# Kernel optimization log

Measured on AMD Instinct MI355X. Metric: run time of the kernel, lower is better.

## Reference

```python
import jax, jax.numpy as jnp
import numpy as np

NEG_SLOPE = 0.2  # DGL GATConv default negative_slope


def gat_layer(x, W, al, ar, b, src, dst):
    """One DGL-style GATConv layer. x:[N,F], W:[F,H*D], al/ar:[H,D], b:[H*D].
    Returns [N,H,D]."""
    N = x.shape[0]
    H, D = al.shape
    feat = (x @ W).reshape(N, H, D)               # projected features
    el = jnp.einsum('nhd,hd->nh', feat, al)       # src attention term
    er = jnp.einsum('nhd,hd->nh', feat, ar)       # dst attention term
    e = jax.nn.leaky_relu(el[src] + er[dst], NEG_SLOPE)   # [E,H]
    # segment softmax over destination nodes
    m = jax.ops.segment_max(e, dst, num_segments=N)       # [N,H]
    m = jnp.where(jnp.isfinite(m), m, 0.0)                # isolated nodes
    ex = jnp.exp(e - m[dst])                              # [E,H]
    denom = jax.ops.segment_sum(ex, dst, num_segments=N)  # [N,H]
    a = ex / denom[dst]                                   # [E,H]
    msg = a[:, :, None] * feat[src]                       # [E,H,D]
    rst = jax.ops.segment_sum(msg, dst, num_segments=N)   # [N,H,D]
    return rst + b.reshape(1, H, D)


def setup_inputs() -> dict:
    key = jax.random.key(0)
    ks = jax.random.split(key, 10)
    N, E = 100000, 1600000
    F_IN, H1, D1, F_OUT = 128, 8, 16, 64
    HID = H1 * D1  # 128
    features = jax.random.normal(ks[0], (N, F_IN), dtype=jnp.float32)
    src = jax.random.randint(ks[1], (E,), 0, N, dtype=jnp.int32)
    dst = jax.random.randint(ks[2], (E,), 0, N, dtype=jnp.int32)
    edge_type = jax.random.randint(ks[3], (E,), 0, 4, dtype=jnp.int32)
    s1 = 1.0 / np.sqrt(F_IN)
    s2 = 1.0 / np.sqrt(HID)
    w1 = jax.random.normal(ks[4], (F_IN, HID), dtype=jnp.float32) * s1
    al1 = jax.random.normal(ks[5], (H1, D1), dtype=jnp.float32) * 0.1
    ar1 = jax.random.normal(ks[6], (H1, D1), dtype=jnp.float32) * 0.1
    b1 = jnp.zeros((HID,), dtype=jnp.float32)
    w2 = jax.random.normal(ks[7], (HID, F_OUT), dtype=jnp.float32) * s2
    al2 = jax.random.normal(ks[8], (1, F_OUT), dtype=jnp.float32) * 0.1
    ar2 = jax.random.normal(ks[9], (1, F_OUT), dtype=jnp.float32) * 0.1
    b2 = jnp.zeros((F_OUT,), dtype=jnp.float32)
    return dict(features=features, src=src, dst=dst, edge_type=edge_type,
                w1=w1, al1=al1, ar1=ar1, b1=b1,
                w2=w2, al2=al2, ar2=ar2, b2=b2)


def reference(features, src, dst, edge_type, w1, al1, ar1, b1, w2, al2, ar2, b2):
    N = features.shape[0]
    # conv1: [N,H,D] -> flatten heads -> relu
    h = gat_layer(features, w1, al1, ar1, b1, src, dst).reshape(N, -1)
    h = jax.nn.relu(h)
    # conv2: single head -> squeeze -> relu
    h = gat_layer(h, w2, al2, ar2, b2, src, dst)[:, 0, :]
    h = jax.nn.relu(h)
    # dot-product edge predictor (u_dot_v) + sigmoid
    score = jnp.einsum('ed,ed->e', h[src], h[dst])
    return jax.nn.sigmoid(score)
```

## Files before the change

kernel.cpp:

```cpp
#include <hip/hip_runtime.h>
#include <math.h>

#define F_IN 128
#define HID 128
#define H1 8
#define D1 16
#define F_OUT 64

#define BSHIFT 7
#define NPB 128
#define CH 4096
#define CAP 4096

typedef unsigned int uint;
typedef unsigned short ushort;

typedef __bf16 bf16x8 __attribute__((ext_vector_type(8)));
typedef float f32x4 __attribute__((ext_vector_type(4)));
typedef float f32x2 __attribute__((ext_vector_type(2)));

__device__ __forceinline__ float bf2f(ushort u) {
  uint v = ((uint)u) << 16;
  return __builtin_bit_cast(float, v);
}
__device__ __forceinline__ ushort f2bf(float f) {
  uint u = __builtin_bit_cast(uint, f);
  u = (u + 0x7FFFu + ((u >> 16) & 1u)) >> 16;
  return (ushort)u;
}
__device__ __forceinline__ f32x2 bfpair(uint w) {
  f32x2 r;
  r.x = __builtin_bit_cast(float, w << 16);
  r.y = __builtin_bit_cast(float, w & 0xFFFF0000u);
  return r;
}


__global__ __launch_bounds__(256) void bucket_scatter(const int* __restrict__ src,
                                                      const int* __restrict__ dst,
                                                      int* __restrict__ bcursor,
                                                      uint* __restrict__ pairs, int E, int nb) {
  __shared__ int cnt_l[1024], base_l[1024], off_l[1024];
  for (int i = threadIdx.x; i < nb; i += 256) { cnt_l[i] = 0; off_l[i] = 0; }
  __syncthreads();
  int e0 = blockIdx.x * CH;
  int t = threadIdx.x;
#pragma unroll 4
  for (int k = 0; k < CH / 256; ++k) {
    int e = e0 + k * 256 + t;
    if (e < E) atomicAdd(&cnt_l[dst[e] >> BSHIFT], 1);
  }
  __syncthreads();
  for (int i = t; i < nb; i += 256)
    base_l[i] = cnt_l[i] ? atomicAdd(&bcursor[i], cnt_l[i]) : 0;
  __syncthreads();
#pragma unroll 4
  for (int k = 0; k < CH / 256; ++k) {
    int e = e0 + k * 256 + t;
    if (e < E) {
      int d = dst[e], b = d >> BSHIFT;
      int o = base_l[b] + atomicAdd(&off_l[b], 1);
      if (o < CAP) pairs[(size_t)b * CAP + o] = ((uint)(d & (NPB - 1)) << 25) | (uint)src[e];
    }
  }
}

__global__ void scan_buckets(const int* __restrict__ bcursor, int* __restrict__ bbase,
                             int nb, int total) {
  __shared__ int sdata[1024];
  int t = threadIdx.x;
  int v = (t < nb) ? bcursor[t] : 0;
  sdata[t] = v;
  __syncthreads();
  for (int off = 1; off < 1024; off <<= 1) {
    int u = (t >= off) ? sdata[t - off] : 0;
    __syncthreads();
    sdata[t] += u;
    __syncthreads();
  }
  if (t < nb) bbase[t] = sdata[t] - v;
  if (t == 0) bbase[nb] = total;
}

__global__ __launch_bounds__(256) void build_csr(const uint* __restrict__ pairs,
                                                 const int* __restrict__ bcursor,
                                                 const int* __restrict__ bbase,
                                                 int* __restrict__ row_ptr,
                                                 int* __restrict__ src_sorted,
                                                 int nn, int total) {
  __shared__ int h[NPB], pref[NPB];
  int b = blockIdx.x, t = threadIdx.x;
  if (t < NPB) h[t] = 0;
  __syncthreads();
  size_t lo = (size_t)b * CAP;
  int cnt = bcursor[b];
  int csr_base = bbase[b];
  for (int e = t; e < cnt; e += 256) atomicAdd(&h[pairs[lo + e] >> 25], 1);
  __syncthreads();
  if (t < NPB) pref[t] = h[t];
  __syncthreads();
  for (int off = 1; off < NPB; off <<= 1) {
    int v = (t >= off && t < NPB) ? pref[t - off] : 0;
    __syncthreads();
    if (t < NPB) pref[t] += v;
    __syncthreads();
  }
  int node_base = b << BSHIFT;
  int nodes = min(NPB, nn - node_base);
  if (t < nodes) {
    int ex = csr_base + pref[t] - h[t];
    row_ptr[node_base + t] = ex;
    h[t] = ex;
  }
  __syncthreads();
  for (int e = t; e < cnt; e += 256) {
    uint p = pairs[lo + e];
    int pos = atomicAdd(&h[p >> 25], 1);
    src_sorted[pos] = (int)(p & 0x1FFFFFFu);
  }
  if (b == 0 && t == 0) row_ptr[nn] = total;
}


template <int COLS, bool ABF16>
__global__ __launch_bounds__(256) void mfma_gemm(const void* __restrict__ Xv,
                                                 const float* __restrict__ W,
                                                 ushort* __restrict__ Y, int nrows) {
  constexpr int NCT = COLS / 16;
  __shared__ ushort wlds[128 * COLS];
  constexpr int ITER = (128 * COLS) / 512;
#pragma unroll
  for (int it = 0; it < ITER; ++it) {
    int idx = it * 512 + (int)threadIdx.x * 2;
    float2 wv = *(const float2*)(W + idx);
    int k = idx / COLS, c = idx % COLS;
    int t = k >> 5, kb = (k >> 3) & 3, j = k & 7;
    wlds[(((t * NCT + (c >> 4)) * 64) + ((c & 15) | (kb << 4))) * 8 + j] = f2bf(wv.x);
    int c1 = c + 1;
    wlds[(((t * NCT + (c1 >> 4)) * 64) + ((c1 & 15) | (kb << 4))) * 8 + j] = f2bf(wv.y);
  }
  __syncthreads();

  int wid = threadIdx.x >> 6, lane = threadIdx.x & 63;
  long r0 = (long)blockIdx.x * 256 + wid * 64;
  if (r0 >= nrows) return;
  int lr = lane & 15, kb = lane >> 4;
  long ar[4];
#pragma unroll
  for (int mi = 0; mi < 4; ++mi) {
    long r = r0 + mi * 16 + lr;
    ar[mi] = (r < nrows) ? r : (long)(nrows - 1);
  }
  f32x4 acc[4][NCT];
#pragma unroll
  for (int mi = 0; mi < 4; ++mi)
#pragma unroll
    for (int ct = 0; ct < NCT; ++ct) acc[mi][ct] = (f32x4){0.f, 0.f, 0.f, 0.f};

#pragma unroll
  for (int t = 0; t < 4; ++t) {
    bf16x8 af[4];
#pragma unroll
    for (int mi = 0; mi < 4; ++mi) {
      if constexpr (ABF16) {
        const ushort* xp = (const ushort*)Xv + ar[mi] * 128 + t * 32 + kb * 8;
        af[mi] = *(const bf16x8*)xp;
      } else {
        const float* xp = (const float*)Xv + ar[mi] * 128 + t * 32 + kb * 8;
        float4 u = *(const float4*)xp;
        float4 v = *(const float4*)(xp + 4);
        bf16x8 a;
        a[0] = (__bf16)u.x; a[1] = (__bf16)u.y; a[2] = (__bf16)u.z; a[3] = (__bf16)u.w;
        a[4] = (__bf16)v.x; a[5] = (__bf16)v.y; a[6] = (__bf16)v.z; a[7] = (__bf16)v.w;
        af[mi] = a;
      }
    }
#pragma unroll
    for (int ct = 0; ct < NCT; ++ct) {
      bf16x8 bf = *(const bf16x8*)&wlds[((t * NCT + ct) * 64 + lane) * 8];
#pragma unroll
      for (int mi = 0; mi < 4; ++mi)
        acc[mi][ct] = __builtin_amdgcn_mfma_f32_16x16x32_bf16(af[mi], bf, acc[mi][ct], 0, 0, 0);
    }
  }

#pragma unroll
  for (int mi = 0; mi < 4; ++mi) {
#pragma unroll
    for (int ct = 0; ct < NCT; ++ct) {
#pragma unroll
      for (int reg = 0; reg < 4; ++reg) {
        long r = r0 + mi * 16 + kb * 4 + reg;
        if (r < nrows) Y[r * COLS + ct * 16 + lr] = f2bf(acc[mi][ct][reg]);
      }
    }
  }
}


__global__ void elr1_kernel(const ushort* __restrict__ feat, const float* __restrict__ al,
                            const float* __restrict__ ar, ushort* __restrict__ el,
                            float* __restrict__ er, int nn) {
  int idx = blockIdx.x * blockDim.x + threadIdx.x;
  if (idx >= nn * H1) return;
  int n = idx >> 3, h = idx & 7;
  const uint4* f4 = (const uint4*)(feat + (size_t)n * HID + h * D1);
  const float* a = al + h * D1;
  const float* r = ar + h * D1;
  float sl = 0.f, sr = 0.f;
#pragma unroll
  for (int j = 0; j < 2; ++j) {
    uint4 v = f4[j];
    uint ws[4] = {v.x, v.y, v.z, v.w};
#pragma unroll
    for (int k = 0; k < 4; ++k) {
      float f0 = bf2f((ushort)(ws[k] & 0xFFFF));
      float f1 = bf2f((ushort)(ws[k] >> 16));
      int d = j * 8 + k * 2;
      sl += f0 * a[d] + f1 * a[d + 1];
      sr += f0 * r[d] + f1 * r[d + 1];
    }
  }
  el[idx] = f2bf(sl);
  er[idx] = sr;
}

__global__ void elr2_kernel(const ushort* __restrict__ feat, const float* __restrict__ al,
                            const float* __restrict__ ar, float* __restrict__ el,
                            float* __restrict__ er, int nn) {
  int n = blockIdx.x * blockDim.x + threadIdx.x;
  if (n >= nn) return;
  const uint4* f4 = (const uint4*)(feat + (size_t)n * F_OUT);
  float sl = 0.f, sr = 0.f;
#pragma unroll
  for (int j = 0; j < 8; ++j) {
    uint4 v = f4[j];
    uint ws[4] = {v.x, v.y, v.z, v.w};
#pragma unroll
    for (int k = 0; k < 4; ++k) {
      float f0 = bf2f((ushort)(ws[k] & 0xFFFF));
      float f1 = bf2f((ushort)(ws[k] >> 16));
      int d = j * 8 + k * 2;
      sl += f0 * al[d] + f1 * al[d + 1];
      sr += f0 * ar[d] + f1 * ar[d + 1];
    }
  }
  el[n] = sl;
  er[n] = sr;
}


template <int H, int D, int VEC, bool EL_BF16>
__global__ __launch_bounds__(256) void agg_kernel(
    const ushort* __restrict__ feat, const void* __restrict__ elv,
    const float* __restrict__ er, const int* __restrict__ row_ptr,
    const int* __restrict__ src_sorted, const float* __restrict__ bias,
    ushort* __restrict__ out, int nn) {
  constexpr int F = H * D;
  constexpr int LPG = 16;
  constexpr int CHUNK = 32;
  static_assert(F == LPG * VEC, "lane layout");
  int w = threadIdx.x >> 6, lane = threadIdx.x & 63;
  int g = lane >> 4, li = lane & 15;
  int n = blockIdx.x * 16 + w * 4 + g;
  __shared__ float p_sh[4][4][H][CHUNK + 2];
  __shared__ int s_sh[4][4][CHUNK + 2];
  bool node_ok = n < nn;
  int start = 0, deg = 0;
  if (node_ok) {
    start = row_ptr[n];
    deg = row_ptr[n + 1] - start;
  }
  int d0 = li * VEC;
  int h = d0 / D;
  float er_reg[H];
#pragma unroll
  for (int q = 0; q < H; ++q) er_reg[q] = 0.f;
  if (node_ok) {
    if constexpr (H == 8) {
      float4 e0 = *(const float4*)(er + (size_t)n * 8);
      float4 e1 = *(const float4*)(er + (size_t)n * 8 + 4);
      er_reg[0] = e0.x; er_reg[1] = e0.y; er_reg[2] = e0.z; er_reg[3] = e0.w;
      er_reg[4] = e1.x; er_reg[5] = e1.y; er_reg[6] = e1.z; er_reg[7] = e1.w;
    } else {
      er_reg[0] = er[n];
    }
  }
  float L = 0.f;
  f32x2 acc2[VEC / 2];
#pragma unroll
  for (int v = 0; v < VEC / 2; ++v) acc2[v] = (f32x2){0.f, 0.f};

  for (int c0 = 0; c0 < deg; c0 += CHUNK) {
    int cnt = min(CHUNK, deg - c0);
    int e0i = c0 + 2 * li;
    int2 s2 = make_int2(0, 0);
    if (e0i + 1 < deg) s2 = *(const int2*)(src_sorted + start + e0i);
    else if (e0i < deg) s2.x = src_sorted[start + e0i];
    *(int2*)&s_sh[w][g][2 * li] = s2;
#pragma unroll
    for (int half = 0; half < 2; ++half) {
      int s = half ? s2.y : s2.x;
      bool valid = (e0i + half) < deg;
      float p8[H];
      if (valid) {
        if constexpr (H == 8) {
          float ev[8];
          if constexpr (EL_BF16) {
            uint4 q4 = *(const uint4*)((const ushort*)elv + (size_t)s * 8);
            uint qs[4] = {q4.x, q4.y, q4.z, q4.w};
#pragma unroll
            for (int k = 0; k < 4; ++k) {
              f32x2 f = bfpair(qs[k]);
              ev[2 * k] = f.x;
              ev[2 * k + 1] = f.y;
            }
          } else {
            float4 e0 = *(const float4*)((const float*)elv + (size_t)s * 8);
            float4 e1 = *(const float4*)((const float*)elv + (size_t)s * 8 + 4);
            ev[0] = e0.x; ev[1] = e0.y; ev[2] = e0.z; ev[3] = e0.w;
            ev[4] = e1.x; ev[5] = e1.y; ev[6] = e1.z; ev[7] = e1.w;
          }
#pragma unroll
          for (int q = 0; q < 8; ++q) {
            float v = ev[q] + er_reg[q];
            v = v > 0.f ? v : 0.2f * v;
            p8[q] = __expf(v);
          }
        } else {
          float v = ((const float*)elv)[s] + er_reg[0];
          v = v > 0.f ? v : 0.2f * v;
          p8[0] = __expf(v);
        }
      } else {
#pragma unroll
        for (int q = 0; q < H; ++q) p8[q] = 0.f;
      }
#pragma unroll
      for (int q = 0; q < H; ++q) p_sh[w][g][q][2 * li + half] = p8[q];
    }
    __builtin_amdgcn_wave_barrier();
    const ushort* fb = feat + d0;
    int j = 0;
    for (; j + 3 < cnt; j += 4) {
      int sa = s_sh[w][g][j], sb = s_sh[w][g][j + 1];
      int sc = s_sh[w][g][j + 2], sd = s_sh[w][g][j + 3];
      float pa = p_sh[w][g][h][j], pb = p_sh[w][g][h][j + 1];
      float pc = p_sh[w][g][h][j + 2], pd = p_sh[w][g][h][j + 3];
      L += pa + pb + pc + pd;
      f32x2 Pa = {pa, pa}, Pb = {pb, pb}, Pc = {pc, pc}, Pd = {pd, pd};
      if constexpr (VEC == 8) {
        uint4 va = *(const uint4*)(fb + (size_t)sa * F);
        uint4 vb = *(const uint4*)(fb + (size_t)sb * F);
        uint4 vc = *(const uint4*)(fb + (size_t)sc * F);
        uint4 vd = *(const uint4*)(fb + (size_t)sd * F);
        uint wa[4] = {va.x, va.y, va.z, va.w};
        uint wb[4] = {vb.x, vb.y, vb.z, vb.w};
        uint wc[4] = {vc.x, vc.y, vc.z, vc.w};
        uint wd[4] = {vd.x, vd.y, vd.z, vd.w};
#pragma unroll
        for (int k = 0; k < 4; ++k) {
          acc2[k] += Pa * bfpair(wa[k]);
          acc2[k] += Pb * bfpair(wb[k]);
          acc2[k] += Pc * bfpair(wc[k]);
          acc2[k] += Pd * bfpair(wd[k]);
        }
      } else {
        uint2 va = *(const uint2*)(fb + (size_t)sa * F);
        uint2 vb = *(const uint2*)(fb + (size_t)sb * F);
        uint2 vc = *(const uint2*)(fb + (size_t)sc * F);
        uint2 vd = *(const uint2*)(fb + (size_t)sd * F);
        acc2[0] += Pa * bfpair(va.x) + Pb * bfpair(vb.x) + Pc * bfpair(vc.x) + Pd * bfpair(vd.x);
        acc2[1] += Pa * bfpair(va.y) + Pb * bfpair(vb.y) + Pc * bfpair(vc.y) + Pd * bfpair(vd.y);
      }
    }
    for (; j < cnt; ++j) {
      float pj = p_sh[w][g][h][j];
      int sj = s_sh[w][g][j];
      L += pj;
      f32x2 Pj = {pj, pj};
      if constexpr (VEC == 8) {
        uint4 v = *(const uint4*)(fb + (size_t)sj * F);
        uint wv[4] = {v.x, v.y, v.z, v.w};
#pragma unroll
        for (int k = 0; k < 4; ++k) acc2[k] += Pj * bfpair(wv[k]);
      } else {
        uint2 v = *(const uint2*)(fb + (size_t)sj * F);
        acc2[0] += Pj * bfpair(v.x);
        acc2[1] += Pj * bfpair(v.y);
      }
    }
    __builtin_amdgcn_wave_barrier();
  }

  if (!node_ok) return;
  float inv = (L > 0.f) ? 1.f / L : 0.f;
  ushort us[VEC];
#pragma unroll
  for (int v = 0; v < VEC / 2; ++v) {
    us[2 * v] = f2bf(fmaxf(acc2[v].x * inv + bias[d0 + 2 * v], 0.f));
    us[2 * v + 1] = f2bf(fmaxf(acc2[v].y * inv + bias[d0 + 2 * v + 1], 0.f));
  }
  if constexpr (VEC == 4) {
    ushort4 u4 = {us[0], us[1], us[2], us[3]};
    *(ushort4*)&out[(size_t)n * F + d0] = u4;
  } else {
    ushort4 u40 = {us[0], us[1], us[2], us[3]};
    ushort4 u41 = {us[4], us[5], us[6], us[7]};
    *(ushort4*)&out[(size_t)n * F + d0] = u40;
    *(ushort4*)&out[(size_t)n * F + d0 + 4] = u41;
  }
}


__global__ void score_kernel(const ushort* __restrict__ h2, const int* __restrict__ src,
                             const int* __restrict__ dst, float* __restrict__ out, int E) {
  int tid = blockIdx.x * blockDim.x + threadIdx.x;
  int e = tid >> 2, sub = tid & 3;
  if (e >= E) return;
  int s = src[e], d = dst[e];
  const ushort* sp = h2 + (size_t)s * F_OUT + sub * 16;
  const ushort* dp = h2 + (size_t)d * F_OUT + sub * 16;
  uint4 a0 = *(const uint4*)sp;
  uint4 a1 = *(const uint4*)(sp + 8);
  uint4 b0 = *(const uint4*)dp;
  uint4 b1 = *(const uint4*)(dp + 8);
  uint aw[8] = {a0.x, a0.y, a0.z, a0.w, a1.x, a1.y, a1.z, a1.w};
  uint bw[8] = {b0.x, b0.y, b0.z, b0.w, b1.x, b1.y, b1.z, b1.w};
  f32x2 acc2 = {0.f, 0.f};
#pragma unroll
  for (int k = 0; k < 8; ++k) acc2 += bfpair(aw[k]) * bfpair(bw[k]);
  float p = acc2.x + acc2.y;
  p += __shfl_xor(p, 1);
  p += __shfl_xor(p, 2);
  if (sub == 0) out[e] = 1.f / (1.f + __expf(-p));
}


extern "C" void kernel_launch(void* const* d_in, const int* in_sizes, int n_in,
                              void* d_out, int out_size, void* d_ws, size_t ws_size,
                              hipStream_t stream) {
  const float* features = (const float*)d_in[0];
  const int* src = (const int*)d_in[1];
  const int* dst = (const int*)d_in[2];
  const float* w1 = (const float*)d_in[4];
  const float* al1 = (const float*)d_in[5];
  const float* ar1 = (const float*)d_in[6];
  const float* b1 = (const float*)d_in[7];
  const float* w2 = (const float*)d_in[8];
  const float* al2 = (const float*)d_in[9];
  const float* ar2 = (const float*)d_in[10];
  const float* b2 = (const float*)d_in[11];
  float* out = (float*)d_out;
  const int N = in_sizes[0] / F_IN;
  const int E = in_sizes[1];

  const int NB = (N + NPB - 1) >> BSHIFT;

  char* ws = (char*)d_ws;
  size_t off = 0;
  auto alloc = [&](size_t bytes) {
    void* p = ws + off;
    off = (off + bytes + 255) & ~(size_t)255;
    return p;
  };
  int* row_ptr = (int*)alloc((size_t)(N + 1) * 4);
  int* src_sorted = (int*)alloc((size_t)E * 4);
  int* bbase = (int*)alloc((size_t)1025 * 4);
  int* bcursor = (int*)alloc((size_t)1024 * 4);
  uint* pairs = (uint*)alloc((size_t)NB * CAP * 4);
  ushort* feat1 = (ushort*)alloc((size_t)N * HID * 2);
  ushort* el1 = (ushort*)alloc((size_t)N * H1 * 2);
  float* er1 = (float*)alloc((size_t)N * H1 * 4);
  ushort* h1b = (ushort*)alloc((size_t)N * HID * 2);
  ushort* h2 = (ushort*)alloc((size_t)N * F_OUT * 2);
  float* el2 = (float*)alloc((size_t)N * 4);
  float* er2 = (float*)alloc((size_t)N * 4);
  ushort* feat2 = feat1;

  hipMemsetAsync(bcursor, 0, (size_t)NB * 4, stream);
  bucket_scatter<<<(E + CH - 1) / CH, 256, 0, stream>>>(src, dst, bcursor, pairs, E, NB);
  scan_buckets<<<1, 1024, 0, stream>>>(bcursor, bbase, NB, E);
  build_csr<<<NB, 256, 0, stream>>>(pairs, bcursor, bbase, row_ptr, src_sorted, N, E);

  const int gblocks = (N + 255) / 256;

  mfma_gemm<HID, false><<<gblocks, 256, 0, stream>>>(features, w1, feat1, N);
  elr1_kernel<<<(N * H1 + 255) / 256, 256, 0, stream>>>(feat1, al1, ar1, el1, er1, N);
  agg_kernel<H1, D1, 8, true><<<(N + 15) / 16, 256, 0, stream>>>(
      feat1, el1, er1, row_ptr, src_sorted, b1, h1b, N);

  mfma_gemm<F_OUT, true><<<gblocks, 256, 0, stream>>>(h1b, w2, feat2, N);
  elr2_kernel<<<(N + 255) / 256, 256, 0, stream>>>(feat2, al2, ar2, el2, er2, N);
  agg_kernel<1, F_OUT, 4, false><<<(N + 15) / 16, 256, 0, stream>>>(
      feat2, el2, er2, row_ptr, src_sorted, b2, h2, N);

  {
    long threads = (long)E * 4;
    int blocks = (int)((threads + 255) / 256);
    score_kernel<<<blocks, 256, 0, stream>>>(h2, src, dst, out, E);
  }
}
```

Measured before the change: 241.9 us.

## Degree-sort node order for aggregation, fuse ELR into GEMM, unroll gathers

Several independent changes land together. The separate bucket scan is folded into build_csr, with each block summing the preceding bucket counts itself. A degree histogram, scan and scatter produce a node order sorted by in-degree, which both aggregation kernels use so that the node groups sharing a wave have similar degrees. Layer 2's el/er attention terms are computed in the GEMM epilogue from fp32 accumulators, removing elr2_kernel and a re-read of feat2. The gather loop is unrolled from 4 to 8 neighbours for more loads in flight. The costs are two extra small kernels, a redundant O(NB) prefix sum in every build_csr block, scattered output writes from permuted nodes, and higher register pressure.

```diff
diff --git a/kernel.cpp b/kernel.cpp
--- a/kernel.cpp
+++ b/kernel.cpp
@@ -65,38 +65,32 @@
   }
 }
 
-__global__ void scan_buckets(const int* __restrict__ bcursor, int* __restrict__ bbase,
-                             int nb, int total) {
-  __shared__ int sdata[1024];
-  int t = threadIdx.x;
-  int v = (t < nb) ? bcursor[t] : 0;
-  sdata[t] = v;
-  __syncthreads();
-  for (int off = 1; off < 1024; off <<= 1) {
-    int u = (t >= off) ? sdata[t - off] : 0;
-    __syncthreads();
-    sdata[t] += u;
-    __syncthreads();
-  }
-  if (t < nb) bbase[t] = sdata[t] - v;
-  if (t == 0) bbase[nb] = total;
-}
-
 __global__ __launch_bounds__(256) void build_csr(const uint* __restrict__ pairs,
                                                  const int* __restrict__ bcursor,
-                                                 const int* __restrict__ bbase,
                                                  int* __restrict__ row_ptr,
                                                  int* __restrict__ src_sorted,
+                                                 int* __restrict__ dhist,
                                                  int nn, int total) {
-  __shared__ int h[NPB], pref[NPB];
+  __shared__ int h[NPB], pref[NPB], red[256];
   int b = blockIdx.x, t = threadIdx.x;
+  int part = 0;
+  for (int i = t; i < b; i += 256) part += bcursor[i];
+  red[t] = part;
+  __syncthreads();
+  for (int off = 128; off > 0; off >>= 1) {
+    if (t < off) red[t] += red[t + off];
+    __syncthreads();
+  }
+  int csr_base = red[0];
   if (t < NPB) h[t] = 0;
   __syncthreads();
   size_t lo = (size_t)b * CAP;
   int cnt = bcursor[b];
-  int csr_base = bbase[b];
   for (int e = t; e < cnt; e += 256) atomicAdd(&h[pairs[lo + e] >> 25], 1);
   __syncthreads();
+  int node_base = b << BSHIFT;
+  int nodes = min(NPB, nn - node_base);
+  if (t < nodes) atomicAdd(&dhist[min(h[t], 511)], 1);
   if (t < NPB) pref[t] = h[t];
   __syncthreads();
   for (int off = 1; off < NPB; off <<= 1) {
@@ -105,8 +99,6 @@
     if (t < NPB) pref[t] += v;
     __syncthreads();
   }
-  int node_base = b << BSHIFT;
-  int nodes = min(NPB, nn - node_base);
   if (t < nodes) {
     int ex = csr_base + pref[t] - h[t];
     row_ptr[node_base + t] = ex;
@@ -121,11 +113,40 @@
   if (b == 0 && t == 0) row_ptr[nn] = total;
 }
 
-
-template <int COLS, bool ABF16>
+__global__ void order_scan(int* __restrict__ dhist) {
+  __shared__ int s[512];
+  int t = threadIdx.x;
+  int v = dhist[t];
+  s[t] = v;
+  __syncthreads();
+  for (int off = 1; off < 512; off <<= 1) {
+    int u = (t >= off) ? s[t - off] : 0;
+    __syncthreads();
+    s[t] += u;
+    __syncthreads();
+  }
+  dhist[t] = s[t] - v;
+}
+
+__global__ __launch_bounds__(256) void order_scatter(const int* __restrict__ row_ptr,
+                                                     int* __restrict__ dcur,
+                                                     int* __restrict__ node_order, int nn) {
+  int n = blockIdx.x * 256 + threadIdx.x;
+  if (n >= nn) return;
+  int deg = row_ptr[n + 1] - row_ptr[n];
+  int pos = atomicAdd(&dcur[min(deg, 511)], 1);
+  node_order[pos] = n;
+}
+
+
+template <int COLS, bool ABF16, bool FUSE_ELR>
 __global__ __launch_bounds__(256) void mfma_gemm(const void* __restrict__ Xv,
                                                  const float* __restrict__ W,
-                                                 ushort* __restrict__ Y, int nrows) {
+                                                 ushort* __restrict__ Y,
+                                                 const float* __restrict__ al,
+                                                 const float* __restrict__ ar,
+                                                 float* __restrict__ el,
+                                                 float* __restrict__ er, int nrows) {
   constexpr int NCT = COLS / 16;
   __shared__ ushort wlds[128 * COLS];
   constexpr int ITER = (128 * COLS) / 512;
@@ -145,11 +166,11 @@
   long r0 = (long)blockIdx.x * 256 + wid * 64;
   if (r0 >= nrows) return;
   int lr = lane & 15, kb = lane >> 4;
-  long ar[4];
+  long ar4[4];
 #pragma unroll
   for (int mi = 0; mi < 4; ++mi) {
     long r = r0 + mi * 16 + lr;
-    ar[mi] = (r < nrows) ? r : (long)(nrows - 1);
+    ar4[mi] = (r < nrows) ? r : (long)(nrows - 1);
   }
   f32x4 acc[4][NCT];
 #pragma unroll
@@ -163,10 +184,10 @@
 #pragma unroll
     for (int mi = 0; mi < 4; ++mi) {
       if constexpr (ABF16) {
-        const ushort* xp = (const ushort*)Xv + ar[mi] * 128 + t * 32 + kb * 8;
+        const ushort* xp = (const ushort*)Xv + ar4[mi] * 128 + t * 32 + kb * 8;
         af[mi] = *(const bf16x8*)xp;
       } else {
-        const float* xp = (const float*)Xv + ar[mi] * 128 + t * 32 + kb * 8;
+        const float* xp = (const float*)Xv + ar4[mi] * 128 + t * 32 + kb * 8;
         float4 u = *(const float4*)xp;
         float4 v = *(const float4*)(xp + 4);
         bf16x8 a;
@@ -192,6 +213,34 @@
       for (int reg = 0; reg < 4; ++reg) {
         long r = r0 + mi * 16 + kb * 4 + reg;
         if (r < nrows) Y[r * COLS + ct * 16 + lr] = f2bf(acc[mi][ct][reg]);
+      }
+    }
+  }
+
+  if constexpr (FUSE_ELR) {
+    float alv[NCT], arv[NCT];
+#pragma unroll
+    for (int ct = 0; ct < NCT; ++ct) {
+      alv[ct] = al[ct * 16 + lr];
+      arv[ct] = ar[ct * 16 + lr];
+    }
+#pragma unroll
+    for (int mi = 0; mi < 4; ++mi) {
+#pragma unroll
+      for (int reg = 0; reg < 4; ++reg) {
+        float pe = 0.f, pr = 0.f;
+#pragma unroll
+        for (int ct = 0; ct < NCT; ++ct) {
+          pe += acc[mi][ct][reg] * alv[ct];
+          pr += acc[mi][ct][reg] * arv[ct];
+        }
+#pragma unroll
+        for (int off = 1; off < 16; off <<= 1) {
+          pe += __shfl_xor(pe, off);
+          pr += __shfl_xor(pr, off);
+        }
+        long r = r0 + mi * 16 + kb * 4 + reg;
+        if (lr == 0 && r < nrows) { el[r] = pe; er[r] = pr; }
       }
     }
   }
@@ -207,46 +256,21 @@
   const uint4* f4 = (const uint4*)(feat + (size_t)n * HID + h * D1);
   const float* a = al + h * D1;
   const float* r = ar + h * D1;
-  float sl = 0.f, sr = 0.f;
+  f32x2 sl2 = {0.f, 0.f}, sr2 = {0.f, 0.f};
 #pragma unroll
   for (int j = 0; j < 2; ++j) {
     uint4 v = f4[j];
     uint ws[4] = {v.x, v.y, v.z, v.w};
 #pragma unroll
     for (int k = 0; k < 4; ++k) {
-      float f0 = bf2f((ushort)(ws[k] & 0xFFFF));
-      float f1 = bf2f((ushort)(ws[k] >> 16));
       int d = j * 8 + k * 2;
-      sl += f0 * a[d] + f1 * a[d + 1];
-      sr += f0 * r[d] + f1 * r[d + 1];
-    }
-  }
-  el[idx] = f2bf(sl);
-  er[idx] = sr;
-}
-
-__global__ void elr2_kernel(const ushort* __restrict__ feat, const float* __restrict__ al,
-                            const float* __restrict__ ar, float* __restrict__ el,
-                            float* __restrict__ er, int nn) {
-  int n = blockIdx.x * blockDim.x + threadIdx.x;
-  if (n >= nn) return;
-  const uint4* f4 = (const uint4*)(feat + (size_t)n * F_OUT);
-  float sl = 0.f, sr = 0.f;
-#pragma unroll
-  for (int j = 0; j < 8; ++j) {
-    uint4 v = f4[j];
-    uint ws[4] = {v.x, v.y, v.z, v.w};
-#pragma unroll
-    for (int k = 0; k < 4; ++k) {
-      float f0 = bf2f((ushort)(ws[k] & 0xFFFF));
-      float f1 = bf2f((ushort)(ws[k] >> 16));
-      int d = j * 8 + k * 2;
-      sl += f0 * al[d] + f1 * al[d + 1];
-      sr += f0 * ar[d] + f1 * ar[d + 1];
-    }
-  }
-  el[n] = sl;
-  er[n] = sr;
+      f32x2 f = bfpair(ws[k]);
+      sl2 += f * *(const f32x2*)(a + d);
+      sr2 += f * *(const f32x2*)(r + d);
+    }
+  }
+  el[idx] = f2bf(sl2.x + sl2.y);
+  er[idx] = sr2.x + sr2.y;
 }
 
 
@@ -254,20 +278,21 @@
 __global__ __launch_bounds__(256) void agg_kernel(
     const ushort* __restrict__ feat, const void* __restrict__ elv,
     const float* __restrict__ er, const int* __restrict__ row_ptr,
-    const int* __restrict__ src_sorted, const float* __restrict__ bias,
-    ushort* __restrict__ out, int nn) {
+    const int* __restrict__ src_sorted, const int* __restrict__ node_order,
+    const float* __restrict__ bias, ushort* __restrict__ out, int nn) {
   constexpr int F = H * D;
   constexpr int LPG = 16;
   constexpr int CHUNK = 32;
   static_assert(F == LPG * VEC, "lane layout");
   int w = threadIdx.x >> 6, lane = threadIdx.x & 63;
   int g = lane >> 4, li = lane & 15;
-  int n = blockIdx.x * 16 + w * 4 + g;
+  int idx = blockIdx.x * 16 + w * 4 + g;
   __shared__ float p_sh[4][4][H][CHUNK + 2];
   __shared__ int s_sh[4][4][CHUNK + 2];
-  bool node_ok = n < nn;
-  int start = 0, deg = 0;
+  bool node_ok = idx < nn;
+  int n = 0, start = 0, deg = 0;
   if (node_ok) {
+    n = node_order[idx];
     start = row_ptr[n];
     deg = row_ptr[n + 1] - start;
   }
@@ -342,36 +367,38 @@
     __builtin_amdgcn_wave_barrier();
     const ushort* fb = feat + d0;
     int j = 0;
-    for (; j + 3 < cnt; j += 4) {
-      int sa = s_sh[w][g][j], sb = s_sh[w][g][j + 1];
-      int sc = s_sh[w][g][j + 2], sd = s_sh[w][g][j + 3];
-      float pa = p_sh[w][g][h][j], pb = p_sh[w][g][h][j + 1];
-      float pc = p_sh[w][g][h][j + 2], pd = p_sh[w][g][h][j + 3];
-      L += pa + pb + pc + pd;
-      f32x2 Pa = {pa, pa}, Pb = {pb, pb}, Pc = {pc, pc}, Pd = {pd, pd};
+    for (; j + 7 < cnt; j += 8) {
+      int sj[8];
+      float pj[8];
+#pragma unroll
+      for (int u = 0; u < 8; ++u) {
+        sj[u] = s_sh[w][g][j + u];
+        pj[u] = p_sh[w][g][h][j + u];
+      }
       if constexpr (VEC == 8) {
-        uint4 va = *(const uint4*)(fb + (size_t)sa * F);
-        uint4 vb = *(const uint4*)(fb + (size_t)sb * F);
-        uint4 vc = *(const uint4*)(fb + (size_t)sc * F);
-        uint4 vd = *(const uint4*)(fb + (size_t)sd * F);
-        uint wa[4] = {va.x, va.y, va.z, va.w};
-        uint wb[4] = {vb.x, vb.y, vb.z, vb.w};
-        uint wc[4] = {vc.x, vc.y, vc.z, vc.w};
-        uint wd[4] = {vd.x, vd.y, vd.z, vd.w};
-#pragma unroll
-        for (int k = 0; k < 4; ++k) {
-          acc2[k] += Pa * bfpair(wa[k]);
-          acc2[k] += Pb * bfpair(wb[k]);
-          acc2[k] += Pc * bfpair(wc[k]);
-          acc2[k] += Pd * bfpair(wd[k]);
+        uint4 vv[8];
+#pragma unroll
+        for (int u = 0; u < 8; ++u) vv[u] = *(const uint4*)(fb + (size_t)sj[u] * F);
+#pragma unroll
+        for (int u = 0; u < 8; ++u) {
+          L += pj[u];
+          f32x2 P = {pj[u], pj[u]};
+          acc2[0] += P * bfpair(vv[u].x);
+          acc2[1] += P * bfpair(vv[u].y);
+          acc2[2] += P * bfpair(vv[u].z);
+          acc2[3] += P * bfpair(vv[u].w);
         }
       } else {
-        uint2 va = *(const uint2*)(fb + (size_t)sa * F);
-        uint2 vb = *(const uint2*)(fb + (size_t)sb * F);
-        uint2 vc = *(const uint2*)(fb + (size_t)sc * F);
-        uint2 vd = *(const uint2*)(fb + (size_t)sd * F);
-        acc2[0] += Pa * bfpair(va.x) + Pb * bfpair(vb.x) + Pc * bfpair(vc.x) + Pd * bfpair(vd.x);
-        acc2[1] += Pa * bfpair(va.y) + Pb * bfpair(vb.y) + Pc * bfpair(vc.y) + Pd * bfpair(vd.y);
+        uint2 vv[8];
+#pragma unroll
+        for (int u = 0; u < 8; ++u) vv[u] = *(const uint2*)(fb + (size_t)sj[u] * F);
+#pragma unroll
+        for (int u = 0; u < 8; ++u) {
+          L += pj[u];
+          f32x2 P = {pj[u], pj[u]};
+          acc2[0] += P * bfpair(vv[u].x);
+          acc2[1] += P * bfpair(vv[u].y);
+        }
       }
     }
     for (; j < cnt; ++j) {
@@ -381,9 +408,10 @@
       f32x2 Pj = {pj, pj};
       if constexpr (VEC == 8) {
         uint4 v = *(const uint4*)(fb + (size_t)sj * F);
-        uint wv[4] = {v.x, v.y, v.z, v.w};
-#pragma unroll
-        for (int k = 0; k < 4; ++k) acc2[k] += Pj * bfpair(wv[k]);
+        acc2[0] += Pj * bfpair(v.x);
+        acc2[1] += Pj * bfpair(v.y);
+        acc2[2] += Pj * bfpair(v.z);
+        acc2[3] += Pj * bfpair(v.w);
       } else {
         uint2 v = *(const uint2*)(fb + (size_t)sj * F);
         acc2[0] += Pj * bfpair(v.x);
@@ -466,8 +494,9 @@
   };
   int* row_ptr = (int*)alloc((size_t)(N + 1) * 4);
   int* src_sorted = (int*)alloc((size_t)E * 4);
-  int* bbase = (int*)alloc((size_t)1025 * 4);
-  int* bcursor = (int*)alloc((size_t)1024 * 4);
+  int* bcursor = (int*)alloc((size_t)1536 * 4);
+  int* dhist = bcursor + 1024;
+  int* node_order = (int*)alloc((size_t)N * 4);
   uint* pairs = (uint*)alloc((size_t)NB * CAP * 4);
   ushort* feat1 = (ushort*)alloc((size_t)N * HID * 2);
   ushort* el1 = (ushort*)alloc((size_t)N * H1 * 2);
@@ -478,22 +507,24 @@
   float* er2 = (float*)alloc((size_t)N * 4);
   ushort* feat2 = feat1;
 
-  hipMemsetAsync(bcursor, 0, (size_t)NB * 4, stream);
+  hipMemsetAsync(bcursor, 0, (size_t)1536 * 4, stream);
   bucket_scatter<<<(E + CH - 1) / CH, 256, 0, stream>>>(src, dst, bcursor, pairs, E, NB);
-  scan_buckets<<<1, 1024, 0, stream>>>(bcursor, bbase, NB, E);
-  build_csr<<<NB, 256, 0, stream>>>(pairs, bcursor, bbase, row_ptr, src_sorted, N, E);
+  build_csr<<<NB, 256, 0, stream>>>(pairs, bcursor, row_ptr, src_sorted, dhist, N, E);
+  order_scan<<<1, 512, 0, stream>>>(dhist);
+  order_scatter<<<(N + 255) / 256, 256, 0, stream>>>(row_ptr, dhist, node_order, N);
 
   const int gblocks = (N + 255) / 256;
 
-  mfma_gemm<HID, false><<<gblocks, 256, 0, stream>>>(features, w1, feat1, N);
+  mfma_gemm<HID, false, false><<<gblocks, 256, 0, stream>>>(
+      features, w1, feat1, nullptr, nullptr, nullptr, nullptr, N);
   elr1_kernel<<<(N * H1 + 255) / 256, 256, 0, stream>>>(feat1, al1, ar1, el1, er1, N);
   agg_kernel<H1, D1, 8, true><<<(N + 15) / 16, 256, 0, stream>>>(
-      feat1, el1, er1, row_ptr, src_sorted, b1, h1b, N);
-
-  mfma_gemm<F_OUT, true><<<gblocks, 256, 0, stream>>>(h1b, w2, feat2, N);
-  elr2_kernel<<<(N + 255) / 256, 256, 0, stream>>>(feat2, al2, ar2, el2, er2, N);
+      feat1, el1, er1, row_ptr, src_sorted, node_order, b1, h1b, N);
+
+  mfma_gemm<F_OUT, true, true><<<gblocks, 256, 0, stream>>>(
+      h1b, w2, feat2, al2, ar2, el2, er2, N);
   agg_kernel<1, F_OUT, 4, false><<<(N + 15) / 16, 256, 0, stream>>>(
-      feat2, el2, er2, row_ptr, src_sorted, b2, h2, N);
+      feat2, el2, er2, row_ptr, src_sorted, node_order, b2, h2, N);
 
   {
     long threads = (long)E * 4;
```

Measured after the change: 766.2 us. 217% more time.
